# Optimization experiments

Measured on AMD Instinct MI355X. Metric: run time of the kernel, lower is better.

The kernel has to match this reference:

```python
import jax, jax.numpy as jnp
import numpy as np

B, S, D = 2, 2048, 512
H = 8
G = 4
LAMBDA_INIT = 0.2  # 0.8 - 0.6*exp(-0.3*(layer_idx-1)) with layer_idx=1
EPS = 1e-5


def setup_inputs() -> dict:
    key = jax.random.key(0)
    ks = jax.random.split(key, 16)
    n = jax.random.normal
    return {
        "x": n(ks[0], (B, S, D), jnp.float32),
        "K1_w": n(ks[1], (D, D), jnp.float32) * 0.02,
        "K1_b": n(ks[2], (D,), jnp.float32) * 0.02,
        "Q1_w": n(ks[3], (D, D), jnp.float32) * 0.02,
        "K2_w": n(ks[4], (D, D), jnp.float32) * 0.02,
        "K2_b": n(ks[5], (D,), jnp.float32) * 0.02,
        "Q2_w": n(ks[6], (D, D), jnp.float32) * 0.02,
        "V_w": n(ks[7], (D, D), jnp.float32) * 0.02,
        "lambda_q1": n(ks[8], (H, 1), jnp.float32),
        "lambda_k1": n(ks[9], (H, 1), jnp.float32),
        "lambda_q2": n(ks[10], (H, 1), jnp.float32),
        "lambda_k2": n(ks[11], (H, 1), jnp.float32),
        "gn_w": jnp.ones((D,), jnp.float32),
        "gn_b": jnp.zeros((D,), jnp.float32),
        "out_w": n(ks[12], (D, D), jnp.float32) * 0.02,
        "out_b": n(ks[13], (D,), jnp.float32) * 0.02,
    }


def reference(x, K1_w, K1_b, Q1_w, K2_w, K2_b, Q2_w, V_w,
              lambda_q1, lambda_k1, lambda_q2, lambda_k2,
              gn_w, gn_b, out_w, out_b):
    b, s, d = x.shape
    hd = d // H

    def heads(t):  # (b,s,d) -> (b,H,s,hd)
        return t.reshape(b, s, H, hd).transpose(0, 2, 1, 3)

    q1 = heads(x @ Q1_w.T)
    k1 = heads(x @ K1_w.T + K1_b)
    q2 = heads(x @ Q2_w.T)
    k2 = heads(x @ K2_w.T + K2_b)
    v = heads(x @ V_w.T)

    scale = hd ** 0.5
    a1 = jax.nn.softmax(jnp.einsum('bhqd,bhkd->bhqk', q1, k1) / scale, axis=-1)
    a2 = jax.nn.softmax(jnp.einsum('bhqd,bhkd->bhqk', q2, k2) / scale, axis=-1)

    lam = (jnp.exp(lambda_q1 * lambda_k1)
           - jnp.exp(lambda_q2 * lambda_k2) + LAMBDA_INIT)  # (H,1)
    attn = a1 - lam.reshape(1, H, 1, 1) * a2

    o = jnp.einsum('bhqk,bhkd->bhqd', attn, v)
    o = o.transpose(0, 2, 1, 3).reshape(b, s, d)

    # GroupNorm over channels: input (b, d, s), groups G normalize over (d/G, s)
    xc = o.transpose(0, 2, 1).reshape(b, G, d // G, s)
    mu = xc.mean(axis=(2, 3), keepdims=True)
    var = xc.var(axis=(2, 3), keepdims=True)
    xn = ((xc - mu) * jax.lax.rsqrt(var + EPS)).reshape(b, d, s)
    xn = xn * gn_w[None, :, None] + gn_b[None, :, None]

    y = xn.transpose(0, 2, 1) @ out_w.T + out_b
    return y
```

## Files before the change

kernel.cpp:

```cpp
#include <hip/hip_runtime.h>
#include <hip/hip_bf16.h>

typedef __bf16 bf16;
typedef __attribute__((ext_vector_type(8))) __bf16 bf16x8;
typedef __attribute__((ext_vector_type(4))) float f32x4;

#define MFMA16(a, b, c) __builtin_amdgcn_mfma_f32_16x16x32_bf16((a), (b), (c), 0, 0, 0)

static constexpr float EPS = 1e-5f;
static constexpr float LAMBDA_INIT = 0.2f;

__device__ __forceinline__ bf16x8 cvt8(const float* p) {
    const f32x4 a = *(const f32x4*)p;
    const f32x4 b = *(const f32x4*)(p + 4);
    bf16x8 r;
    r[0] = (bf16)a[0]; r[1] = (bf16)a[1]; r[2] = (bf16)a[2]; r[3] = (bf16)a[3];
    r[4] = (bf16)b[0]; r[5] = (bf16)b[1]; r[6] = (bf16)b[2]; r[7] = (bf16)b[3];
    return r;
}

__device__ __forceinline__ void gload_lds16(const void* g, void* l) {
    __builtin_amdgcn_global_load_lds(
        (const __attribute__((address_space(1))) unsigned int*)g,
        (__attribute__((address_space(3))) unsigned int*)l,
        16, 0, 0);
}

__global__ __launch_bounds__(256) void prep_kernel(
    const float* __restrict__ x,
    const float* __restrict__ q1w, const float* __restrict__ k1w,
    const float* __restrict__ q2w, const float* __restrict__ k2w,
    const float* __restrict__ vw,
    const float* __restrict__ ow, const float* __restrict__ gnw,
    const float* __restrict__ gnb,
    bf16* __restrict__ xb, bf16* __restrict__ wb,
    bf16* __restrict__ owg, float* __restrict__ S0, float* __restrict__ stats)
{
    const int tid = threadIdx.x;
    if (blockIdx.x < 1664) {
        const size_t base = ((size_t)blockIdx.x * 256 + tid) * 8;
        if (base < 2097152) {
            *(bf16x8*)(xb + base) = cvt8(x + base);
        } else {
            const size_t wbase = base - 2097152;
            const int wsel = (int)(wbase >> 18);
            const size_t off = wbase & 262143;
            const float* W = (wsel == 0) ? q1w : (wsel == 1) ? k1w :
                             (wsel == 2) ? q2w : (wsel == 3) ? k2w : vw;
            *(bf16x8*)(wb + wbase) = cvt8(W + off);
        }
        return;
    }

    __shared__ float red[4];
    const int pb = blockIdx.x - 1664;
    if (pb == 0 && tid < 16) stats[tid] = 0.f;

    const int n0 = pb * 16;
    const int c0 = tid, c1 = tid + 256;
    const float gw0 = gnw[c0], gw1 = gnw[c1];
    const float gb0 = gnb[c0], gb1 = gnb[c1];

    for (int n = 0; n < 16; ++n) {
        const size_t rowb = (size_t)(n0 + n) * 512;
        const float w0 = ow[rowb + c0];
        const float w1 = ow[rowb + c1];
        owg[rowb + c0] = (bf16)(w0 * gw0);
        owg[rowb + c1] = (bf16)(w1 * gw1);
        float s = gb0 * w0 + gb1 * w1;
#pragma unroll
        for (int off = 1; off < 64; off <<= 1) s += __shfl_xor(s, off, 64);
        if ((tid & 63) == 0) red[tid >> 6] = s;
        __syncthreads();
        if (tid == 0) S0[n0 + n] = red[0] + red[1] + red[2] + red[3];
        __syncthreads();
    }
}

__global__ __launch_bounds__(256) void proj_kernel(
    const bf16* __restrict__ xb, const bf16* __restrict__ wb,
    const float* __restrict__ k1b, const float* __restrict__ k2b,
    bf16* __restrict__ q1o, bf16* __restrict__ k1o,
    bf16* __restrict__ q2o, bf16* __restrict__ k2o,
    bf16* __restrict__ vto)
{
    __shared__ __align__(16) bf16 As[128 * 32];
    __shared__ __align__(16) bf16 Bs[128 * 32];

    const int tid = threadIdx.x;
    const int wave = tid >> 6, lane = tid & 63;
    const int l15 = lane & 15, quad = lane >> 4;
    const int wm = wave >> 1, wn = wave & 1;

    const int mb = blockIdx.x / 20;
    const int nb = blockIdx.x % 20;
    const int wsel = nb >> 2;
    const int nrow0 = (nb & 3) * 128;

    const int srow = lane >> 2;
    const int scol = (lane & 3) * 8;
    const bf16* ag = xb + (size_t)(mb * 128 + srow) * 512 + scol;
    const bf16* bg = wb + (size_t)(wsel * 512 + nrow0 + srow) * 512 + scol;

    f32x4 acc[4][4];
#pragma unroll
    for (int i = 0; i < 4; ++i)
#pragma unroll
        for (int j = 0; j < 4; ++j)
            acc[i][j] = (f32x4){0.f, 0.f, 0.f, 0.f};

    for (int k0 = 0; k0 < 512; k0 += 32) {
#pragma unroll
        for (int c = 0; c < 2; ++c) {
            const int chunk = wave * 2 + c;
            gload_lds16(ag + (size_t)(chunk * 16) * 512 + k0, As + chunk * 512);
            gload_lds16(bg + (size_t)(chunk * 16) * 512 + k0, Bs + chunk * 512);
        }
        __syncthreads();

        bf16x8 af[4], bfr[4];
#pragma unroll
        for (int i = 0; i < 4; ++i)
            af[i] = *(const bf16x8*)(As + (wm * 64 + i * 16 + l15) * 32 + quad * 8);
#pragma unroll
        for (int j = 0; j < 4; ++j)
            bfr[j] = *(const bf16x8*)(Bs + (wn * 64 + j * 16 + l15) * 32 + quad * 8);

#pragma unroll
        for (int i = 0; i < 4; ++i)
#pragma unroll
            for (int j = 0; j < 4; ++j)
                acc[i][j] = MFMA16(af[i], bfr[j], acc[i][j]);

        __syncthreads();
    }

    const float scale = (wsel == 0 || wsel == 2) ? 0.125f : 1.0f;
#pragma unroll
    for (int j = 0; j < 4; ++j) {
        const int ncol = nrow0 + wn * 64 + j * 16 + l15;
        float bias = 0.f;
        if (wsel == 1) bias = k1b[ncol];
        if (wsel == 3) bias = k2b[ncol];
        const int h = ncol >> 6, hd = ncol & 63;
#pragma unroll
        for (int i = 0; i < 4; ++i) {
#pragma unroll
            for (int r = 0; r < 4; ++r) {
                const int m = mb * 128 + wm * 64 + i * 16 + quad * 4 + r;
                const int bidx = m >> 11, s = m & 2047;
                const float v = acc[i][j][r] * scale + bias;
                if (wsel == 4) {
                    const int s5 = s & 31;
                    const int p = ((s5 & 15) >> 2) * 8 + (s5 & 3) + ((s5 >> 4) << 2);
                    const int sp = (s & ~31) | p;
                    vto[((size_t)(bidx * 8 + h) * 64 + hd) * 2048 + sp] = (bf16)v;
                } else {
                    bf16* dst = (wsel == 0) ? q1o : (wsel == 1) ? k1o :
                                (wsel == 2) ? q2o : k2o;
                    dst[((size_t)(bidx * 8 + h) * 2048 + s) * 64 + hd] = (bf16)v;
                }
            }
        }
    }
}

__global__ __launch_bounds__(512, 4) void attn_kernel(
    const bf16* __restrict__ q1, const bf16* __restrict__ k1,
    const bf16* __restrict__ q2, const bf16* __restrict__ k2,
    const bf16* __restrict__ vt,
    const float* __restrict__ lq1, const float* __restrict__ lk1,
    const float* __restrict__ lq2, const float* __restrict__ lk2,
    bf16* __restrict__ o, float* __restrict__ stats)
{
    __shared__ __align__(16) bf16 smem[12288];
    __shared__ float lbuf[8][2][16];
    __shared__ float sred[8][2];

    const int tid = threadIdx.x;
    const int wave = tid >> 6;
    const int lane = tid & 63;
    const int l15 = lane & 15, quad = lane >> 4;
    const int qtile = wave & 3;
    const int kg = wave >> 2;

    const int bh = blockIdx.x >> 5;
    const int qt = blockIdx.x & 31;
    const int b = bh >> 3, h = bh & 7;

    const bf16* k1t = k1 + (size_t)bh * 2048 * 64;
    const bf16* k2t = k2 + (size_t)bh * 2048 * 64;
    const bf16* vtt = vt + (size_t)bh * 64 * 2048;

    const int qrow = qt * 64 + qtile * 16 + l15;
    const bf16* q1p = q1 + ((size_t)bh * 2048 + qrow) * 64 + quad * 8;
    const bf16* q2p = q2 + ((size_t)bh * 2048 + qrow) * 64 + quad * 8;
    const bf16x8 q1f0 = *(const bf16x8*)(q1p);
    const bf16x8 q1f1 = *(const bf16x8*)(q1p + 32);
    const bf16x8 q2f0 = *(const bf16x8*)(q2p);
    const bf16x8 q2f1 = *(const bf16x8*)(q2p + 32);

    const int sw = wave & 3;
    const int skey0 = (wave < 4) ? 0 : 1024;
    bf16* k1dst = smem + wave * 512;
    bf16* k2dst = smem + 4096 + wave * 512;
    bf16* vdst  = smem + 8192 + wave * 512;
    const size_t ksrc0 = (size_t)(skey0 + sw * 8 + (lane >> 3)) * 64
                       + 8 * ((lane & 7) ^ (lane >> 3));
    const size_t vsrc0 = (size_t)(sw * 16 + (lane >> 2)) * 2048 + skey0 + (lane & 3) * 8;

    const bf16* k1r = smem + kg * 2048;
    const bf16* k2r = smem + 4096 + kg * 2048;
    const bf16* vr  = smem + 8192 + kg * 2048;

    const int koffa = 8 * (quad ^ (l15 & 7));
    const int koffb = 8 * ((quad + 4) ^ (l15 & 7));

    f32x4 O1[4], O2[4];
    float l1 = 0.f, l2 = 0.f;
#pragma unroll
    for (int t = 0; t < 4; ++t) {
        O1[t] = (f32x4){0.f, 0.f, 0.f, 0.f};
        O2[t] = (f32x4){0.f, 0.f, 0.f, 0.f};
    }

    for (int it = 0; it < 32; ++it) {
        const size_t koff = ksrc0 + (size_t)it * 32 * 64;
        gload_lds16(k1t + koff, k1dst);
        gload_lds16(k2t + koff, k2dst);
        gload_lds16(vtt + vsrc0 + it * 32, vdst);
        __syncthreads();

        const bf16x8 k1t0a = *(const bf16x8*)(k1r + l15 * 64 + koffa);
        const bf16x8 k1t0b = *(const bf16x8*)(k1r + l15 * 64 + koffb);
        const bf16x8 k1t1a = *(const bf16x8*)(k1r + (16 + l15) * 64 + koffa);
        const bf16x8 k1t1b = *(const bf16x8*)(k1r + (16 + l15) * 64 + koffb);
        const bf16x8 k2t0a = *(const bf16x8*)(k2r + l15 * 64 + koffa);
        const bf16x8 k2t0b = *(const bf16x8*)(k2r + l15 * 64 + koffb);
        const bf16x8 k2t1a = *(const bf16x8*)(k2r + (16 + l15) * 64 + koffa);
        const bf16x8 k2t1b = *(const bf16x8*)(k2r + (16 + l15) * 64 + koffb);
        const bf16x8 v0 = *(const bf16x8*)(vr + l15 * 32 + quad * 8);
        const bf16x8 v1 = *(const bf16x8*)(vr + (16 + l15) * 32 + quad * 8);
        const bf16x8 v2 = *(const bf16x8*)(vr + (32 + l15) * 32 + quad * 8);
        const bf16x8 v3 = *(const bf16x8*)(vr + (48 + l15) * 32 + quad * 8);

        f32x4 z = (f32x4){0.f, 0.f, 0.f, 0.f};
        f32x4 s1t0 = MFMA16(k1t0a, q1f0, z);  s1t0 = MFMA16(k1t0b, q1f1, s1t0);
        f32x4 s1t1 = MFMA16(k1t1a, q1f0, z);  s1t1 = MFMA16(k1t1b, q1f1, s1t1);
        f32x4 s2t0 = MFMA16(k2t0a, q2f0, z);  s2t0 = MFMA16(k2t0b, q2f1, s2t0);
        f32x4 s2t1 = MFMA16(k2t1a, q2f0, z);  s2t1 = MFMA16(k2t1b, q2f1, s2t1);

        bf16x8 b1, b2;
#pragma unroll
        for (int r = 0; r < 4; ++r) {
            float e;
            e = __expf(s1t0[r]); l1 += e; b1[r]     = (bf16)e;
            e = __expf(s1t1[r]); l1 += e; b1[4 + r] = (bf16)e;
            e = __expf(s2t0[r]); l2 += e; b2[r]     = (bf16)e;
            e = __expf(s2t1[r]); l2 += e; b2[4 + r] = (bf16)e;
        }

        O1[0] = MFMA16(v0, b1, O1[0]);
        O1[1] = MFMA16(v1, b1, O1[1]);
        O1[2] = MFMA16(v2, b1, O1[2]);
        O1[3] = MFMA16(v3, b1, O1[3]);
        O2[0] = MFMA16(v0, b2, O2[0]);
        O2[1] = MFMA16(v1, b2, O2[1]);
        O2[2] = MFMA16(v2, b2, O2[2]);
        O2[3] = MFMA16(v3, b2, O2[3]);

        __syncthreads();
    }

    l1 += __shfl_xor(l1, 16, 64);  l1 += __shfl_xor(l1, 32, 64);
    l2 += __shfl_xor(l2, 16, 64);  l2 += __shfl_xor(l2, 32, 64);
    if (lane < 16) {
        lbuf[wave][0][lane] = l1;
        lbuf[wave][1][lane] = l2;
    }
    __syncthreads();

    f32x4* rb = (f32x4*)smem;
    if (wave == 4 || wave == 5) {
        f32x4* dst = rb + (wave - 4) * 512;
#pragma unroll
        for (int t = 0; t < 4; ++t) {
            dst[t * 64 + lane]       = O1[t];
            dst[(4 + t) * 64 + lane] = O2[t];
        }
    }
    __syncthreads();
    if (wave == 0 || wave == 1) {
        const f32x4* src = rb + wave * 512;
#pragma unroll
        for (int t = 0; t < 4; ++t) {
            O1[t] += src[t * 64 + lane];
            O2[t] += src[(4 + t) * 64 + lane];
        }
    }
    __syncthreads();
    if (wave == 6 || wave == 7) {
        f32x4* dst = rb + (wave - 6) * 512;
#pragma unroll
        for (int t = 0; t < 4; ++t) {
            dst[t * 64 + lane]       = O1[t];
            dst[(4 + t) * 64 + lane] = O2[t];
        }
    }
    __syncthreads();
    if (wave == 2 || wave == 3) {
        const f32x4* src = rb + (wave - 2) * 512;
#pragma unroll
        for (int t = 0; t < 4; ++t) {
            O1[t] += src[t * 64 + lane];
            O2[t] += src[(4 + t) * 64 + lane];
        }
    }

    float ssum = 0.f, ssq = 0.f;
    if (wave < 4) {
        const float L1 = l1 + lbuf[wave + 4][0][l15];
        const float L2 = l2 + lbuf[wave + 4][1][l15];
        const float lam = __expf(lq1[h] * lk1[h]) - __expf(lq2[h] * lk2[h]) + LAMBDA_INIT;
        const float inv1 = 1.f / L1;
        const float inv2 = lam / L2;
        const size_t row = (size_t)(b * 2048 + qt * 64 + wave * 16 + l15) * 512 + h * 64;
#pragma unroll
        for (int t = 0; t < 4; ++t) {
#pragma unroll
            for (int r = 0; r < 4; ++r) {
                const float val = O1[t][r] * inv1 - O2[t][r] * inv2;
                ssum += val;
                ssq += val * val;
                o[row + t * 16 + quad * 4 + r] = (bf16)val;
            }
        }
    }
#pragma unroll
    for (int off = 1; off < 64; off <<= 1) {
        ssum += __shfl_xor(ssum, off, 64);
        ssq += __shfl_xor(ssq, off, 64);
    }
    if (lane == 0) { sred[wave][0] = ssum; sred[wave][1] = ssq; }
    __syncthreads();
    if (tid == 0) {
        float s0 = 0.f, s1 = 0.f;
        for (int w = 0; w < 8; ++w) { s0 += sred[w][0]; s1 += sred[w][1]; }
        const int bg = b * 4 + (h >> 1);
        atomicAdd(&stats[bg * 2], s0);
        atomicAdd(&stats[bg * 2 + 1], s1);
    }
}

__global__ __launch_bounds__(256) void out_gemm_kernel(
    const bf16* __restrict__ o, const bf16* __restrict__ owg,
    const float* __restrict__ S0, const float* __restrict__ stats,
    const float* __restrict__ ob, float* __restrict__ y)
{
    __shared__ __align__(16) bf16 As[64 * 32];
    __shared__ __align__(16) bf16 Bs[64 * 32];

    const int tid = threadIdx.x;
    const int wave = tid >> 6, lane = tid & 63;
    const int l15 = lane & 15, quad = lane >> 4;

    const int mb = blockIdx.x >> 3;
    const int nb = blockIdx.x & 7;
    const int b = mb >> 5;

    const float N = 128.f * 2048.f;
    float mu[4], rs[4];
#pragma unroll
    for (int g = 0; g < 4; ++g) {
        const float m = stats[(b * 4 + g) * 2] / N;
        const float var = stats[(b * 4 + g) * 2 + 1] / N - m * m;
        mu[g] = m;
        rs[g] = rsqrtf(var + EPS);
    }

    const int srow = wave * 16 + (lane >> 2);
    const int scol = (lane & 3) * 8;
    const bf16* ag = o + (size_t)(mb * 64 + srow) * 512 + scol;
    const bf16* bg = owg + (size_t)(nb * 64 + srow) * 512 + scol;
    bf16* adst = As + wave * 512;
    bf16* bdst = Bs + wave * 512;

    f32x4 acc[4], tot[4];
#pragma unroll
    for (int i = 0; i < 4; ++i) {
        acc[i] = (f32x4){0.f, 0.f, 0.f, 0.f};
        tot[i] = (f32x4){0.f, 0.f, 0.f, 0.f};
    }
    float s1g[4];
    float s1p = 0.f;
#pragma unroll
    for (int g = 0; g < 4; ++g) s1g[g] = 0.f;

    for (int kk = 0; kk < 16; ++kk) {
        gload_lds16(ag + kk * 32, adst);
        gload_lds16(bg + kk * 32, bdst);
        __syncthreads();

        bf16x8 af[4];
#pragma unroll
        for (int i = 0; i < 4; ++i)
            af[i] = *(const bf16x8*)(As + (i * 16 + l15) * 32 + quad * 8);
        const bf16x8 bf = *(const bf16x8*)(Bs + (wave * 16 + l15) * 32 + quad * 8);

#pragma unroll
        for (int i = 0; i < 4; ++i)
            acc[i] = MFMA16(af[i], bf, acc[i]);

#pragma unroll
        for (int j = 0; j < 8; ++j) s1p += (float)bf[j];

        __syncthreads();

        if ((kk & 3) == 3) {
            const int g = kk >> 2;
#pragma unroll
            for (int i = 0; i < 4; ++i) {
#pragma unroll
                for (int r = 0; r < 4; ++r) tot[i][r] += rs[g] * acc[i][r];
                acc[i] = (f32x4){0.f, 0.f, 0.f, 0.f};
            }
            float sg = s1p + __shfl_xor(s1p, 16, 64);
            sg += __shfl_xor(sg, 32, 64);
            s1g[g] = sg;
            s1p = 0.f;
        }
    }

    const int ncol = nb * 64 + wave * 16 + l15;
    float bias = S0[ncol] + ob[ncol];
#pragma unroll
    for (int g = 0; g < 4; ++g) bias -= mu[g] * rs[g] * s1g[g];

#pragma unroll
    for (int i = 0; i < 4; ++i) {
#pragma unroll
        for (int r = 0; r < 4; ++r) {
            const int m = mb * 64 + i * 16 + quad * 4 + r;
            y[(size_t)m * 512 + ncol] = tot[i][r] + bias;
        }
    }
}

extern "C" void kernel_launch(void* const* d_in, const int* in_sizes, int n_in,
                              void* d_out, int out_size, void* d_ws, size_t ws_size,
                              hipStream_t stream)
{
    const float* x   = (const float*)d_in[0];
    const float* K1w = (const float*)d_in[1];
    const float* K1b = (const float*)d_in[2];
    const float* Q1w = (const float*)d_in[3];
    const float* K2w = (const float*)d_in[4];
    const float* K2b = (const float*)d_in[5];
    const float* Q2w = (const float*)d_in[6];
    const float* Vw  = (const float*)d_in[7];
    const float* lq1 = (const float*)d_in[8];
    const float* lk1 = (const float*)d_in[9];
    const float* lq2 = (const float*)d_in[10];
    const float* lk2 = (const float*)d_in[11];
    const float* gnw = (const float*)d_in[12];
    const float* gnb = (const float*)d_in[13];
    const float* Ow  = (const float*)d_in[14];
    const float* Ob  = (const float*)d_in[15];

    const size_t SZ = (size_t)2 * 8 * 2048 * 64;
    bf16* q1 = (bf16*)d_ws;
    bf16* k1 = q1 + SZ;
    bf16* q2 = k1 + SZ;
    bf16* k2 = q2 + SZ;
    bf16* vt = k2 + SZ;
    bf16* o  = vt + SZ;
    bf16* xb = o;
    bf16* wb = o + SZ;
    bf16* owg = wb + (size_t)2560 * 512;
    float* S0 = (float*)(owg + 512 * 512);
    float* stats = S0 + 512;

    prep_kernel<<<1696, 256, 0, stream>>>(x, Q1w, K1w, Q2w, K2w, Vw,
                                          Ow, gnw, gnb, xb, wb, owg, S0, stats);
    proj_kernel<<<640, 256, 0, stream>>>(xb, wb, K1b, K2b,
                                         q1, k1, q2, k2, vt);
    attn_kernel<<<512, 512, 0, stream>>>(q1, k1, q2, k2, vt,
                                         lq1, lk1, lq2, lk2, o, stats);
    out_gemm_kernel<<<512, 256, 0, stream>>>(o, owg, S0, stats, Ob,
                                             (float*)d_out);
}
```

Baseline: 190.2 us.

## Fuse four kernels into one persistent kernel with atomic grid barriers

Merges the prep, projection, attention and output GEMM kernels into a single 512-block, 512-thread kernel. The stages are separated by software grid-wide barriers built on atomic counters, which are reset by a memset before the launch. This is meant to remove three kernel-launch gaps and their tail drain. In exchange the projection GEMM is reshaped to 8 waves with 128 tiles spread over 512 blocks, so some blocks do two tiles, and half the waves sit idle in the output GEMM. The barriers assume all 512 blocks are resident at once; otherwise the kernel deadlocks.

After: 456.3 us. +139.9%, slower.

```diff
diff --git a/kernel.cpp b/kernel.cpp
--- a/kernel.cpp
+++ b/kernel.cpp
@@ -9,6 +9,7 @@
 
 static constexpr float EPS = 1e-5f;
 static constexpr float LAMBDA_INIT = 0.2f;
+static constexpr unsigned NBLK = 512;
 
 __device__ __forceinline__ bf16x8 cvt8(const float* p) {
     const f32x4 a = *(const f32x4*)p;
@@ -26,422 +27,407 @@
         16, 0, 0);
 }
 
-__global__ __launch_bounds__(256) void prep_kernel(
+__device__ __forceinline__ void grid_sync(unsigned* cnt) {
+    __syncthreads();
+    if (threadIdx.x == 0) {
+        __threadfence();
+        __hip_atomic_fetch_add(cnt, 1u, __ATOMIC_ACQ_REL, __HIP_MEMORY_SCOPE_AGENT);
+        while (__hip_atomic_load(cnt, __ATOMIC_ACQUIRE, __HIP_MEMORY_SCOPE_AGENT) < NBLK)
+            __builtin_amdgcn_s_sleep(8);
+        __threadfence();
+    }
+    __syncthreads();
+}
+
+__global__ __launch_bounds__(512, 4) void mega_kernel(
     const float* __restrict__ x,
     const float* __restrict__ q1w, const float* __restrict__ k1w,
     const float* __restrict__ q2w, const float* __restrict__ k2w,
     const float* __restrict__ vw,
+    const float* __restrict__ k1b, const float* __restrict__ k2b,
+    const float* __restrict__ lq1, const float* __restrict__ lk1,
+    const float* __restrict__ lq2, const float* __restrict__ lk2,
     const float* __restrict__ ow, const float* __restrict__ gnw,
-    const float* __restrict__ gnb,
+    const float* __restrict__ gnb, const float* __restrict__ ob,
     bf16* __restrict__ xb, bf16* __restrict__ wb,
-    bf16* __restrict__ owg, float* __restrict__ S0, float* __restrict__ stats)
+    bf16* __restrict__ q1, bf16* __restrict__ k1,
+    bf16* __restrict__ q2, bf16* __restrict__ k2,
+    bf16* __restrict__ vt, bf16* __restrict__ o,
+    bf16* __restrict__ owg, float* __restrict__ S0,
+    float* __restrict__ stats, unsigned* __restrict__ bar,
+    float* __restrict__ y)
 {
+    __shared__ __align__(16) bf16 smem[12288];
+    __shared__ float lbuf[8][2][16];
+    __shared__ float sred[8][2];
+
     const int tid = threadIdx.x;
-    if (blockIdx.x < 1664) {
-        const size_t base = ((size_t)blockIdx.x * 256 + tid) * 8;
-        if (base < 2097152) {
+    const int wave = tid >> 6;
+    const int lane = tid & 63;
+    const int l15 = lane & 15, quad = lane >> 4;
+
+    {
+        const unsigned gtid = blockIdx.x * 512 + tid;
+        {
+            const size_t base = (size_t)gtid * 8;
             *(bf16x8*)(xb + base) = cvt8(x + base);
-        } else {
-            const size_t wbase = base - 2097152;
+        }
+        if (gtid < 163840u) {
+            const size_t wbase = (size_t)gtid * 8;
             const int wsel = (int)(wbase >> 18);
             const size_t off = wbase & 262143;
             const float* W = (wsel == 0) ? q1w : (wsel == 1) ? k1w :
                              (wsel == 2) ? q2w : (wsel == 3) ? k2w : vw;
             *(bf16x8*)(wb + wbase) = cvt8(W + off);
         }
-        return;
+        const int n = blockIdx.x;
+        const float w = ow[(size_t)n * 512 + tid];
+        owg[(size_t)n * 512 + tid] = (bf16)(w * gnw[tid]);
+        float s = gnb[tid] * w;
+#pragma unroll
+        for (int off = 1; off < 64; off <<= 1) s += __shfl_xor(s, off, 64);
+        if (lane == 0) sred[wave][0] = s;
+        __syncthreads();
+        if (tid == 0) {
+            float t0 = 0.f;
+            for (int wv = 0; wv < 8; ++wv) t0 += sred[wv][0];
+            S0[n] = t0;
+        }
+        if (blockIdx.x == 0 && tid < 16) stats[tid] = 0.f;
     }
-
-    __shared__ float red[4];
-    const int pb = blockIdx.x - 1664;
-    if (pb == 0 && tid < 16) stats[tid] = 0.f;
-
-    const int n0 = pb * 16;
-    const int c0 = tid, c1 = tid + 256;
-    const float gw0 = gnw[c0], gw1 = gnw[c1];
-    const float gb0 = gnb[c0], gb1 = gnb[c1];
-
-    for (int n = 0; n < 16; ++n) {
-        const size_t rowb = (size_t)(n0 + n) * 512;
-        const float w0 = ow[rowb + c0];
-        const float w1 = ow[rowb + c1];
-        owg[rowb + c0] = (bf16)(w0 * gw0);
-        owg[rowb + c1] = (bf16)(w1 * gw1);
-        float s = gb0 * w0 + gb1 * w1;
-#pragma unroll
-        for (int off = 1; off < 64; off <<= 1) s += __shfl_xor(s, off, 64);
-        if ((tid & 63) == 0) red[tid >> 6] = s;
-        __syncthreads();
-        if (tid == 0) S0[n0 + n] = red[0] + red[1] + red[2] + red[3];
-        __syncthreads();
+    grid_sync(bar + 0);
+
+    {
+        bf16* As = smem;
+        bf16* Bs = smem + 4096;
+        const int wm = wave >> 2, wn = wave & 3;
+        const int srow = lane >> 2;
+        const int scol = (lane & 3) * 8;
+
+        for (int t = blockIdx.x; t < 640; t += 512) {
+            const int mb = t / 20;
+            const int nb = t % 20;
+            const int wsel = nb >> 2;
+            const int nrow0 = (nb & 3) * 128;
+
+            const bf16* ag = xb + (size_t)(mb * 128 + srow) * 512 + scol;
+            const bf16* bg = wb + (size_t)(wsel * 512 + nrow0 + srow) * 512 + scol;
+
+            f32x4 acc[4][2];
+#pragma unroll
+            for (int i = 0; i < 4; ++i)
+#pragma unroll
+                for (int j = 0; j < 2; ++j)
+                    acc[i][j] = (f32x4){0.f, 0.f, 0.f, 0.f};
+
+            for (int k0 = 0; k0 < 512; k0 += 32) {
+                gload_lds16(ag + (size_t)(wave * 16) * 512 + k0, As + wave * 512);
+                gload_lds16(bg + (size_t)(wave * 16) * 512 + k0, Bs + wave * 512);
+                __syncthreads();
+
+                bf16x8 af[4], bfr[2];
+#pragma unroll
+                for (int i = 0; i < 4; ++i)
+                    af[i] = *(const bf16x8*)(As + (wm * 64 + i * 16 + l15) * 32 + quad * 8);
+#pragma unroll
+                for (int j = 0; j < 2; ++j)
+                    bfr[j] = *(const bf16x8*)(Bs + (wn * 32 + j * 16 + l15) * 32 + quad * 8);
+
+#pragma unroll
+                for (int i = 0; i < 4; ++i)
+#pragma unroll
+                    for (int j = 0; j < 2; ++j)
+                        acc[i][j] = MFMA16(af[i], bfr[j], acc[i][j]);
+
+                __syncthreads();
+            }
+
+            const float scale = (wsel == 0 || wsel == 2) ? 0.125f : 1.0f;
+#pragma unroll
+            for (int j = 0; j < 2; ++j) {
+                const int ncol = nrow0 + wn * 32 + j * 16 + l15;
+                float bias = 0.f;
+                if (wsel == 1) bias = k1b[ncol];
+                if (wsel == 3) bias = k2b[ncol];
+                const int h = ncol >> 6, hd = ncol & 63;
+#pragma unroll
+                for (int i = 0; i < 4; ++i) {
+#pragma unroll
+                    for (int r = 0; r < 4; ++r) {
+                        const int m = mb * 128 + wm * 64 + i * 16 + quad * 4 + r;
+                        const int bidx = m >> 11, s = m & 2047;
+                        const float v = acc[i][j][r] * scale + bias;
+                        if (wsel == 4) {
+                            const int s5 = s & 31;
+                            const int p = ((s5 & 15) >> 2) * 8 + (s5 & 3) + ((s5 >> 4) << 2);
+                            const int sp = (s & ~31) | p;
+                            vt[((size_t)(bidx * 8 + h) * 64 + hd) * 2048 + sp] = (bf16)v;
+                        } else {
+                            bf16* dst = (wsel == 0) ? q1 : (wsel == 1) ? k1 :
+                                        (wsel == 2) ? q2 : k2;
+                            dst[((size_t)(bidx * 8 + h) * 2048 + s) * 64 + hd] = (bf16)v;
+                        }
+                    }
+                }
+            }
+        }
     }
-}
-
-__global__ __launch_bounds__(256) void proj_kernel(
-    const bf16* __restrict__ xb, const bf16* __restrict__ wb,
-    const float* __restrict__ k1b, const float* __restrict__ k2b,
-    bf16* __restrict__ q1o, bf16* __restrict__ k1o,
-    bf16* __restrict__ q2o, bf16* __restrict__ k2o,
-    bf16* __restrict__ vto)
-{
-    __shared__ __align__(16) bf16 As[128 * 32];
-    __shared__ __align__(16) bf16 Bs[128 * 32];
-
-    const int tid = threadIdx.x;
-    const int wave = tid >> 6, lane = tid & 63;
-    const int l15 = lane & 15, quad = lane >> 4;
-    const int wm = wave >> 1, wn = wave & 1;
-
-    const int mb = blockIdx.x / 20;
-    const int nb = blockIdx.x % 20;
-    const int wsel = nb >> 2;
-    const int nrow0 = (nb & 3) * 128;
-
-    const int srow = lane >> 2;
-    const int scol = (lane & 3) * 8;
-    const bf16* ag = xb + (size_t)(mb * 128 + srow) * 512 + scol;
-    const bf16* bg = wb + (size_t)(wsel * 512 + nrow0 + srow) * 512 + scol;
-
-    f32x4 acc[4][4];
-#pragma unroll
-    for (int i = 0; i < 4; ++i)
-#pragma unroll
-        for (int j = 0; j < 4; ++j)
-            acc[i][j] = (f32x4){0.f, 0.f, 0.f, 0.f};
-
-    for (int k0 = 0; k0 < 512; k0 += 32) {
-#pragma unroll
-        for (int c = 0; c < 2; ++c) {
-            const int chunk = wave * 2 + c;
-            gload_lds16(ag + (size_t)(chunk * 16) * 512 + k0, As + chunk * 512);
-            gload_lds16(bg + (size_t)(chunk * 16) * 512 + k0, Bs + chunk * 512);
-        }
-        __syncthreads();
-
-        bf16x8 af[4], bfr[4];
-#pragma unroll
-        for (int i = 0; i < 4; ++i)
-            af[i] = *(const bf16x8*)(As + (wm * 64 + i * 16 + l15) * 32 + quad * 8);
-#pragma unroll
-        for (int j = 0; j < 4; ++j)
-            bfr[j] = *(const bf16x8*)(Bs + (wn * 64 + j * 16 + l15) * 32 + quad * 8);
-
-#pragma unroll
-        for (int i = 0; i < 4; ++i)
-#pragma unroll
-            for (int j = 0; j < 4; ++j)
-                acc[i][j] = MFMA16(af[i], bfr[j], acc[i][j]);
-
-        __syncthreads();
+    grid_sync(bar + 1);
+
+    {
+        const int qtile = wave & 3;
+        const int kg = wave >> 2;
+        const int bh = blockIdx.x >> 5;
+        const int qt = blockIdx.x & 31;
+        const int b = bh >> 3, h = bh & 7;
+
+        const bf16* k1t = k1 + (size_t)bh * 2048 * 64;
+        const bf16* k2t = k2 + (size_t)bh * 2048 * 64;
+        const bf16* vtt = vt + (size_t)bh * 64 * 2048;
+
+        const int qrow = qt * 64 + qtile * 16 + l15;
+        const bf16* q1p = q1 + ((size_t)bh * 2048 + qrow) * 64 + quad * 8;
+        const bf16* q2p = q2 + ((size_t)bh * 2048 + qrow) * 64 + quad * 8;
+        const bf16x8 q1f0 = *(const bf16x8*)(q1p);
+        const bf16x8 q1f1 = *(const bf16x8*)(q1p + 32);
+        const bf16x8 q2f0 = *(const bf16x8*)(q2p);
+        const bf16x8 q2f1 = *(const bf16x8*)(q2p + 32);
+
+        const int sw = wave & 3;
+        const int skey0 = (wave < 4) ? 0 : 1024;
+        bf16* k1dst = smem + wave * 512;
+        bf16* k2dst = smem + 4096 + wave * 512;
+        bf16* vdst  = smem + 8192 + wave * 512;
+        const size_t ksrc0 = (size_t)(skey0 + sw * 8 + (lane >> 3)) * 64
+                           + 8 * ((lane & 7) ^ (lane >> 3));
+        const size_t vsrc0 = (size_t)(sw * 16 + (lane >> 2)) * 2048 + skey0 + (lane & 3) * 8;
+
+        const bf16* k1r = smem + kg * 2048;
+        const bf16* k2r = smem + 4096 + kg * 2048;
+        const bf16* vr  = smem + 8192 + kg * 2048;
+        const int koffa = 8 * (quad ^ (l15 & 7));
+        const int koffb = 8 * ((quad + 4) ^ (l15 & 7));
+
+        f32x4 O1[4], O2[4];
+        float l1 = 0.f, l2 = 0.f;
+#pragma unroll
+        for (int t = 0; t < 4; ++t) {
+            O1[t] = (f32x4){0.f, 0.f, 0.f, 0.f};
+            O2[t] = (f32x4){0.f, 0.f, 0.f, 0.f};
+        }
+
+        for (int it = 0; it < 32; ++it) {
+            const size_t koff = ksrc0 + (size_t)it * 32 * 64;
+            gload_lds16(k1t + koff, k1dst);
+            gload_lds16(k2t + koff, k2dst);
+            gload_lds16(vtt + vsrc0 + it * 32, vdst);
+            __syncthreads();
+
+            const bf16x8 k1t0a = *(const bf16x8*)(k1r + l15 * 64 + koffa);
+            const bf16x8 k1t0b = *(const bf16x8*)(k1r + l15 * 64 + koffb);
+            const bf16x8 k1t1a = *(const bf16x8*)(k1r + (16 + l15) * 64 + koffa);
+            const bf16x8 k1t1b = *(const bf16x8*)(k1r + (16 + l15) * 64 + koffb);
+            const bf16x8 k2t0a = *(const bf16x8*)(k2r + l15 * 64 + koffa);
+            const bf16x8 k2t0b = *(const bf16x8*)(k2r + l15 * 64 + koffb);
+            const bf16x8 k2t1a = *(const bf16x8*)(k2r + (16 + l15) * 64 + koffa);
+            const bf16x8 k2t1b = *(const bf16x8*)(k2r + (16 + l15) * 64 + koffb);
+            const bf16x8 v0 = *(const bf16x8*)(vr + l15 * 32 + quad * 8);
+            const bf16x8 v1 = *(const bf16x8*)(vr + (16 + l15) * 32 + quad * 8);
+            const bf16x8 v2 = *(const bf16x8*)(vr + (32 + l15) * 32 + quad * 8);
+            const bf16x8 v3 = *(const bf16x8*)(vr + (48 + l15) * 32 + quad * 8);
+
+            f32x4 z = (f32x4){0.f, 0.f, 0.f, 0.f};
+            f32x4 s1t0 = MFMA16(k1t0a, q1f0, z);  s1t0 = MFMA16(k1t0b, q1f1, s1t0);
+            f32x4 s1t1 = MFMA16(k1t1a, q1f0, z);  s1t1 = MFMA16(k1t1b, q1f1, s1t1);
+            f32x4 s2t0 = MFMA16(k2t0a, q2f0, z);  s2t0 = MFMA16(k2t0b, q2f1, s2t0);
+            f32x4 s2t1 = MFMA16(k2t1a, q2f0, z);  s2t1 = MFMA16(k2t1b, q2f1, s2t1);
+
+            bf16x8 b1, b2;
+#pragma unroll
+            for (int r = 0; r < 4; ++r) {
+                float e;
+                e = __expf(s1t0[r]); l1 += e; b1[r]     = (bf16)e;
+                e = __expf(s1t1[r]); l1 += e; b1[4 + r] = (bf16)e;
+                e = __expf(s2t0[r]); l2 += e; b2[r]     = (bf16)e;
+                e = __expf(s2t1[r]); l2 += e; b2[4 + r] = (bf16)e;
+            }
+
+            O1[0] = MFMA16(v0, b1, O1[0]);
+            O1[1] = MFMA16(v1, b1, O1[1]);
+            O1[2] = MFMA16(v2, b1, O1[2]);
+            O1[3] = MFMA16(v3, b1, O1[3]);
+            O2[0] = MFMA16(v0, b2, O2[0]);
+            O2[1] = MFMA16(v1, b2, O2[1]);
+            O2[2] = MFMA16(v2, b2, O2[2]);
+            O2[3] = MFMA16(v3, b2, O2[3]);
+
+            __syncthreads();
+        }
+
+        l1 += __shfl_xor(l1, 16, 64);  l1 += __shfl_xor(l1, 32, 64);
+        l2 += __shfl_xor(l2, 16, 64);  l2 += __shfl_xor(l2, 32, 64);
+        if (lane < 16) {
+            lbuf[wave][0][lane] = l1;
+            lbuf[wave][1][lane] = l2;
+        }
+        __syncthreads();
+
+        f32x4* rb = (f32x4*)smem;
+        if (wave == 4 || wave == 5) {
+            f32x4* dst = rb + (wave - 4) * 512;
+#pragma unroll
+            for (int t = 0; t < 4; ++t) {
+                dst[t * 64 + lane]       = O1[t];
+                dst[(4 + t) * 64 + lane] = O2[t];
+            }
+        }
+        __syncthreads();
+        if (wave == 0 || wave == 1) {
+            const f32x4* src = rb + wave * 512;
+#pragma unroll
+            for (int t = 0; t < 4; ++t) {
+                O1[t] += src[t * 64 + lane];
+                O2[t] += src[(4 + t) * 64 + lane];
+            }
+        }
+        __syncthreads();
+        if (wave == 6 || wave == 7) {
+            f32x4* dst = rb + (wave - 6) * 512;
+#pragma unroll
+            for (int t = 0; t < 4; ++t) {
+                dst[t * 64 + lane]       = O1[t];
+                dst[(4 + t) * 64 + lane] = O2[t];
+            }
+        }
+        __syncthreads();
+        if (wave == 2 || wave == 3) {
+            const f32x4* src = rb + (wave - 2) * 512;
+#pragma unroll
+            for (int t = 0; t < 4; ++t) {
+                O1[t] += src[t * 64 + lane];
+                O2[t] += src[(4 + t) * 64 + lane];
+            }
+        }
+
+        float ssum = 0.f, ssq = 0.f;
+        if (wave < 4) {
+            const float L1 = l1 + lbuf[wave + 4][0][l15];
+            const float L2 = l2 + lbuf[wave + 4][1][l15];
+            const float lam = __expf(lq1[h] * lk1[h]) - __expf(lq2[h] * lk2[h]) + LAMBDA_INIT;
+            const float inv1 = 1.f / L1;
+            const float inv2 = lam / L2;
+            const size_t row = (size_t)(b * 2048 + qt * 64 + wave * 16 + l15) * 512 + h * 64;
+#pragma unroll
+            for (int t = 0; t < 4; ++t) {
+#pragma unroll
+                for (int r = 0; r < 4; ++r) {
+                    const float val = O1[t][r] * inv1 - O2[t][r] * inv2;
+                    ssum += val;
+                    ssq += val * val;
+                    o[row + t * 16 + quad * 4 + r] = (bf16)val;
+                }
+            }
+        }
+#pragma unroll
+        for (int off = 1; off < 64; off <<= 1) {
+            ssum += __shfl_xor(ssum, off, 64);
+            ssq += __shfl_xor(ssq, off, 64);
+        }
+        if (lane == 0) { sred[wave][0] = ssum; sred[wave][1] = ssq; }
+        __syncthreads();
+        if (tid == 0) {
+            float s0 = 0.f, s1 = 0.f;
+            for (int wv = 0; wv < 8; ++wv) { s0 += sred[wv][0]; s1 += sred[wv][1]; }
+            const int bg = b * 4 + (h >> 1);
+            atomicAdd(&stats[bg * 2], s0);
+            atomicAdd(&stats[bg * 2 + 1], s1);
+        }
     }
-
-    const float scale = (wsel == 0 || wsel == 2) ? 0.125f : 1.0f;
-#pragma unroll
-    for (int j = 0; j < 4; ++j) {
-        const int ncol = nrow0 + wn * 64 + j * 16 + l15;
-        float bias = 0.f;
-        if (wsel == 1) bias = k1b[ncol];
-        if (wsel == 3) bias = k2b[ncol];
-        const int h = ncol >> 6, hd = ncol & 63;
+    grid_sync(bar + 2);
+
+    {
+        bf16* As = smem;
+        bf16* Bs = smem + 2048;
+        const int mb = blockIdx.x >> 3;
+        const int nb = blockIdx.x & 7;
+        const int b = mb >> 5;
+
+        const float N = 128.f * 2048.f;
+        float mu[4], rs[4];
+#pragma unroll
+        for (int g = 0; g < 4; ++g) {
+            const float m = stats[(b * 4 + g) * 2] / N;
+            const float var = stats[(b * 4 + g) * 2 + 1] / N - m * m;
+            mu[g] = m;
+            rs[g] = rsqrtf(var + EPS);
+        }
+
+        const int srow = wave * 16 + (lane >> 2);
+        const int scol = (lane & 3) * 8;
+        const bf16* ag = o + (size_t)(mb * 64 + srow) * 512 + scol;
+        const bf16* bg = owg + (size_t)(nb * 64 + srow) * 512 + scol;
+        bf16* adst = As + wave * 512;
+        bf16* bdst = Bs + wave * 512;
+
+        f32x4 acc[4], tot[4];
 #pragma unroll
         for (int i = 0; i < 4; ++i) {
-#pragma unroll
-            for (int r = 0; r < 4; ++r) {
-                const int m = mb * 128 + wm * 64 + i * 16 + quad * 4 + r;
-                const int bidx = m >> 11, s = m & 2047;
-                const float v = acc[i][j][r] * scale + bias;
-                if (wsel == 4) {
-                    const int s5 = s & 31;
-                    const int p = ((s5 & 15) >> 2) * 8 + (s5 & 3) + ((s5 >> 4) << 2);
-                    const int sp = (s & ~31) | p;
-                    vto[((size_t)(bidx * 8 + h) * 64 + hd) * 2048 + sp] = (bf16)v;
-                } else {
-                    bf16* dst = (wsel == 0) ? q1o : (wsel == 1) ? k1o :
-                                (wsel == 2) ? q2o : k2o;
-                    dst[((size_t)(bidx * 8 + h) * 2048 + s) * 64 + hd] = (bf16)v;
+            acc[i] = (f32x4){0.f, 0.f, 0.f, 0.f};
+            tot[i] = (f32x4){0.f, 0.f, 0.f, 0.f};
+        }
+        float s1g[4] = {0.f, 0.f, 0.f, 0.f};
+        float s1p = 0.f;
+
+        for (int kk = 0; kk < 16; ++kk) {
+            if (wave < 4) {
+                gload_lds16(ag + kk * 32, adst);
+                gload_lds16(bg + kk * 32, bdst);
+            }
+            __syncthreads();
+
+            if (wave < 4) {
+                bf16x8 af[4];
+#pragma unroll
+                for (int i = 0; i < 4; ++i)
+                    af[i] = *(const bf16x8*)(As + (i * 16 + l15) * 32 + quad * 8);
+                const bf16x8 bfv = *(const bf16x8*)(Bs + (wave * 16 + l15) * 32 + quad * 8);
+
+#pragma unroll
+                for (int i = 0; i < 4; ++i)
+                    acc[i] = MFMA16(af[i], bfv, acc[i]);
+#pragma unroll
+                for (int j = 0; j < 8; ++j) s1p += (float)bfv[j];
+            }
+            __syncthreads();
+
+            if (wave < 4 && (kk & 3) == 3) {
+                const int g = kk >> 2;
+#pragma unroll
+                for (int i = 0; i < 4; ++i) {
+#pragma unroll
+                    for (int r = 0; r < 4; ++r) tot[i][r] += rs[g] * acc[i][r];
+                    acc[i] = (f32x4){0.f, 0.f, 0.f, 0.f};
                 }
-            }
-        }
-    }
-}
-
-__global__ __launch_bounds__(512, 4) void attn_kernel(
-    const bf16* __restrict__ q1, const bf16* __restrict__ k1,
-    const bf16* __restrict__ q2, const bf16* __restrict__ k2,
-    const bf16* __restrict__ vt,
-    const float* __restrict__ lq1, const float* __restrict__ lk1,
-    const float* __restrict__ lq2, const float* __restrict__ lk2,
-    bf16* __restrict__ o, float* __restrict__ stats)
-{
-    __shared__ __align__(16) bf16 smem[12288];
-    __shared__ float lbuf[8][2][16];
-    __shared__ float sred[8][2];
-
-    const int tid = threadIdx.x;
-    const int wave = tid >> 6;
-    const int lane = tid & 63;
-    const int l15 = lane & 15, quad = lane >> 4;
-    const int qtile = wave & 3;
-    const int kg = wave >> 2;
-
-    const int bh = blockIdx.x >> 5;
-    const int qt = blockIdx.x & 31;
-    const int b = bh >> 3, h = bh & 7;
-
-    const bf16* k1t = k1 + (size_t)bh * 2048 * 64;
-    const bf16* k2t = k2 + (size_t)bh * 2048 * 64;
-    const bf16* vtt = vt + (size_t)bh * 64 * 2048;
-
-    const int qrow = qt * 64 + qtile * 16 + l15;
-    const bf16* q1p = q1 + ((size_t)bh * 2048 + qrow) * 64 + quad * 8;
-    const bf16* q2p = q2 + ((size_t)bh * 2048 + qrow) * 64 + quad * 8;
-    const bf16x8 q1f0 = *(const bf16x8*)(q1p);
-    const bf16x8 q1f1 = *(const bf16x8*)(q1p + 32);
-    const bf16x8 q2f0 = *(const bf16x8*)(q2p);
-    const bf16x8 q2f1 = *(const bf16x8*)(q2p + 32);
-
-    const int sw = wave & 3;
-    const int skey0 = (wave < 4) ? 0 : 1024;
-    bf16* k1dst = smem + wave * 512;
-    bf16* k2dst = smem + 4096 + wave * 512;
-    bf16* vdst  = smem + 8192 + wave * 512;
-    const size_t ksrc0 = (size_t)(skey0 + sw * 8 + (lane >> 3)) * 64
-                       + 8 * ((lane & 7) ^ (lane >> 3));
-    const size_t vsrc0 = (size_t)(sw * 16 + (lane >> 2)) * 2048 + skey0 + (lane & 3) * 8;
-
-    const bf16* k1r = smem + kg * 2048;
-    const bf16* k2r = smem + 4096 + kg * 2048;
-    const bf16* vr  = smem + 8192 + kg * 2048;
-
-    const int koffa = 8 * (quad ^ (l15 & 7));
-    const int koffb = 8 * ((quad + 4) ^ (l15 & 7));
-
-    f32x4 O1[4], O2[4];
-    float l1 = 0.f, l2 = 0.f;
-#pragma unroll
-    for (int t = 0; t < 4; ++t) {
-        O1[t] = (f32x4){0.f, 0.f, 0.f, 0.f};
-        O2[t] = (f32x4){0.f, 0.f, 0.f, 0.f};
-    }
-
-    for (int it = 0; it < 32; ++it) {
-        const size_t koff = ksrc0 + (size_t)it * 32 * 64;
-        gload_lds16(k1t + koff, k1dst);
-        gload_lds16(k2t + koff, k2dst);
-        gload_lds16(vtt + vsrc0 + it * 32, vdst);
-        __syncthreads();
-
-        const bf16x8 k1t0a = *(const bf16x8*)(k1r + l15 * 64 + koffa);
-        const bf16x8 k1t0b = *(const bf16x8*)(k1r + l15 * 64 + koffb);
-        const bf16x8 k1t1a = *(const bf16x8*)(k1r + (16 + l15) * 64 + koffa);
-        const bf16x8 k1t1b = *(const bf16x8*)(k1r + (16 + l15) * 64 + koffb);
-        const bf16x8 k2t0a = *(const bf16x8*)(k2r + l15 * 64 + koffa);
-        const bf16x8 k2t0b = *(const bf16x8*)(k2r + l15 * 64 + koffb);
-        const bf16x8 k2t1a = *(const bf16x8*)(k2r + (16 + l15) * 64 + koffa);
-        const bf16x8 k2t1b = *(const bf16x8*)(k2r + (16 + l15) * 64 + koffb);
-        const bf16x8 v0 = *(const bf16x8*)(vr + l15 * 32 + quad * 8);
-        const bf16x8 v1 = *(const bf16x8*)(vr + (16 + l15) * 32 + quad * 8);
-        const bf16x8 v2 = *(const bf16x8*)(vr + (32 + l15) * 32 + quad * 8);
-        const bf16x8 v3 = *(const bf16x8*)(vr + (48 + l15) * 32 + quad * 8);
-
-        f32x4 z = (f32x4){0.f, 0.f, 0.f, 0.f};
-        f32x4 s1t0 = MFMA16(k1t0a, q1f0, z);  s1t0 = MFMA16(k1t0b, q1f1, s1t0);
-        f32x4 s1t1 = MFMA16(k1t1a, q1f0, z);  s1t1 = MFMA16(k1t1b, q1f1, s1t1);
-        f32x4 s2t0 = MFMA16(k2t0a, q2f0, z);  s2t0 = MFMA16(k2t0b, q2f1, s2t0);
-        f32x4 s2t1 = MFMA16(k2t1a, q2f0, z);  s2t1 = MFMA16(k2t1b, q2f1, s2t1);
-
-        bf16x8 b1, b2;
-#pragma unroll
-        for (int r = 0; r < 4; ++r) {
-            float e;
-            e = __expf(s1t0[r]); l1 += e; b1[r]     = (bf16)e;
-            e = __expf(s1t1[r]); l1 += e; b1[4 + r] = (bf16)e;
-            e = __expf(s2t0[r]); l2 += e; b2[r]     = (bf16)e;
-            e = __expf(s2t1[r]); l2 += e; b2[4 + r] = (bf16)e;
-        }
-
-        O1[0] = MFMA16(v0, b1, O1[0]);
-        O1[1] = MFMA16(v1, b1, O1[1]);
-        O1[2] = MFMA16(v2, b1, O1[2]);
-        O1[3] = MFMA16(v3, b1, O1[3]);
-        O2[0] = MFMA16(v0, b2, O2[0]);
-        O2[1] = MFMA16(v1, b2, O2[1]);
-        O2[2] = MFMA16(v2, b2, O2[2]);
-        O2[3] = MFMA16(v3, b2, O2[3]);
-
-        __syncthreads();
-    }
-
-    l1 += __shfl_xor(l1, 16, 64);  l1 += __shfl_xor(l1, 32, 64);
-    l2 += __shfl_xor(l2, 16, 64);  l2 += __shfl_xor(l2, 32, 64);
-    if (lane < 16) {
-        lbuf[wave][0][lane] = l1;
-        lbuf[wave][1][lane] = l2;
-    }
-    __syncthreads();
-
-    f32x4* rb = (f32x4*)smem;
-    if (wave == 4 || wave == 5) {
-        f32x4* dst = rb + (wave - 4) * 512;
-#pragma unroll
-        for (int t = 0; t < 4; ++t) {
-            dst[t * 64 + lane]       = O1[t];
-            dst[(4 + t) * 64 + lane] = O2[t];
-        }
-    }
-    __syncthreads();
-    if (wave == 0 || wave == 1) {
-        const f32x4* src = rb + wave * 512;
-#pragma unroll
-        for (int t = 0; t < 4; ++t) {
-            O1[t] += src[t * 64 + lane];
-            O2[t] += src[(4 + t) * 64 + lane];
-        }
-    }
-    __syncthreads();
-    if (wave == 6 || wave == 7) {
-        f32x4* dst = rb + (wave - 6) * 512;
-#pragma unroll
-        for (int t = 0; t < 4; ++t) {
-            dst[t * 64 + lane]       = O1[t];
-            dst[(4 + t) * 64 + lane] = O2[t];
-        }
-    }
-    __syncthreads();
-    if (wave == 2 || wave == 3) {
-        const f32x4* src = rb + (wave - 2) * 512;
-#pragma unroll
-        for (int t = 0; t < 4; ++t) {
-            O1[t] += src[t * 64 + lane];
-            O2[t] += src[(4 + t) * 64 + lane];
-        }
-    }
-
-    float ssum = 0.f, ssq = 0.f;
-    if (wave < 4) {
-        const float L1 = l1 + lbuf[wave + 4][0][l15];
-        const float L2 = l2 + lbuf[wave + 4][1][l15];
-        const float lam = __expf(lq1[h] * lk1[h]) - __expf(lq2[h] * lk2[h]) + LAMBDA_INIT;
-        const float inv1 = 1.f / L1;
-        const float inv2 = lam / L2;
-        const size_t row = (size_t)(b * 2048 + qt * 64 + wave * 16 + l15) * 512 + h * 64;
-#pragma unroll
-        for (int t = 0; t < 4; ++t) {
-#pragma unroll
-            for (int r = 0; r < 4; ++r) {
-                const float val = O1[t][r] * inv1 - O2[t][r] * inv2;
-                ssum += val;
-                ssq += val * val;
-                o[row + t * 16 + quad * 4 + r] = (bf16)val;
-            }
-        }
-    }
-#pragma unroll
-    for (int off = 1; off < 64; off <<= 1) {
-        ssum += __shfl_xor(ssum, off, 64);
-        ssq += __shfl_xor(ssq, off, 64);
-    }
-    if (lane == 0) { sred[wave][0] = ssum; sred[wave][1] = ssq; }
-    __syncthreads();
-    if (tid == 0) {
-        float s0 = 0.f, s1 = 0.f;
-        for (int w = 0; w < 8; ++w) { s0 += sred[w][0]; s1 += sred[w][1]; }
-        const int bg = b * 4 + (h >> 1);
-        atomicAdd(&stats[bg * 2], s0);
-        atomicAdd(&stats[bg * 2 + 1], s1);
-    }
-}
-
-__global__ __launch_bounds__(256) void out_gemm_kernel(
-    const bf16* __restrict__ o, const bf16* __restrict__ owg,
-    const float* __restrict__ S0, const float* __restrict__ stats,
-    const float* __restrict__ ob, float* __restrict__ y)
-{
-    __shared__ __align__(16) bf16 As[64 * 32];
-    __shared__ __align__(16) bf16 Bs[64 * 32];
-
-    const int tid = threadIdx.x;
-    const int wave = tid >> 6, lane = tid & 63;
-    const int l15 = lane & 15, quad = lane >> 4;
-
-    const int mb = blockIdx.x >> 3;
-    const int nb = blockIdx.x & 7;
-    const int b = mb >> 5;
-
-    const float N = 128.f * 2048.f;
-    float mu[4], rs[4];
-#pragma unroll
-    for (int g = 0; g < 4; ++g) {
-        const float m = stats[(b * 4 + g) * 2] / N;
-        const float var = stats[(b * 4 + g) * 2 + 1] / N - m * m;
-        mu[g] = m;
-        rs[g] = rsqrtf(var + EPS);
-    }
-
-    const int srow = wave * 16 + (lane >> 2);
-    const int scol = (lane & 3) * 8;
-    const bf16* ag = o + (size_t)(mb * 64 + srow) * 512 + scol;
-    const bf16* bg = owg + (size_t)(nb * 64 + srow) * 512 + scol;
-    bf16* adst = As + wave * 512;
-    bf16* bdst = Bs + wave * 512;
-
-    f32x4 acc[4], tot[4];
-#pragma unroll
-    for (int i = 0; i < 4; ++i) {
-        acc[i] = (f32x4){0.f, 0.f, 0.f, 0.f};
-        tot[i] = (f32x4){0.f, 0.f, 0.f, 0.f};
-    }
-    float s1g[4];
-    float s1p = 0.f;
-#pragma unroll
-    for (int g = 0; g < 4; ++g) s1g[g] = 0.f;
-
-    for (int kk = 0; kk < 16; ++kk) {
-        gload_lds16(ag + kk * 32, adst);
-        gload_lds16(bg + kk * 32, bdst);
-        __syncthreads();
-
-        bf16x8 af[4];
-#pragma unroll
-        for (int i = 0; i < 4; ++i)
-            af[i] = *(const bf16x8*)(As + (i * 16 + l15) * 32 + quad * 8);
-        const bf16x8 bf = *(const bf16x8*)(Bs + (wave * 16 + l15) * 32 + quad * 8);
-
-#pragma unroll
-        for (int i = 0; i < 4; ++i)
-            acc[i] = MFMA16(af[i], bf, acc[i]);
-
-#pragma unroll
-        for (int j = 0; j < 8; ++j) s1p += (float)bf[j];
-
-        __syncthreads();
-
-        if ((kk & 3) == 3) {
-            const int g = kk >> 2;
+                float sg = s1p + __shfl_xor(s1p, 16, 64);
+                sg += __shfl_xor(sg, 32, 64);
+                s1g[g] = sg;
+                s1p = 0.f;
+            }
+        }
+
+        if (wave < 4) {
+            const int ncol = nb * 64 + wave * 16 + l15;
+            float bias = S0[ncol] + ob[ncol];
+#pragma unroll
+            for (int g = 0; g < 4; ++g) bias -= mu[g] * rs[g] * s1g[g];
 #pragma unroll
             for (int i = 0; i < 4; ++i) {
 #pragma unroll
-                for (int r = 0; r < 4; ++r) tot[i][r] += rs[g] * acc[i][r];
-                acc[i] = (f32x4){0.f, 0.f, 0.f, 0.f};
-            }
-            float sg = s1p + __shfl_xor(s1p, 16, 64);
-            sg += __shfl_xor(sg, 32, 64);
-            s1g[g] = sg;
-            s1p = 0.f;
-        }
-    }
-
-    const int ncol = nb * 64 + wave * 16 + l15;
-    float bias = S0[ncol] + ob[ncol];
-#pragma unroll
-    for (int g = 0; g < 4; ++g) bias -= mu[g] * rs[g] * s1g[g];
-
-#pragma unroll
-    for (int i = 0; i < 4; ++i) {
-#pragma unroll
-        for (int r = 0; r < 4; ++r) {
-            const int m = mb * 64 + i * 16 + quad * 4 + r;
-            y[(size_t)m * 512 + ncol] = tot[i][r] + bias;
+                for (int r = 0; r < 4; ++r) {
+                    const int m = mb * 64 + i * 16 + quad * 4 + r;
+                    y[(size_t)m * 512 + ncol] = tot[i][r] + bias;
+                }
+            }
         }
     }
 }
@@ -479,13 +465,12 @@
     bf16* owg = wb + (size_t)2560 * 512;
     float* S0 = (float*)(owg + 512 * 512);
     float* stats = S0 + 512;
-
-    prep_kernel<<<1696, 256, 0, stream>>>(x, Q1w, K1w, Q2w, K2w, Vw,
-                                          Ow, gnw, gnb, xb, wb, owg, S0, stats);
-    proj_kernel<<<640, 256, 0, stream>>>(xb, wb, K1b, K2b,
-                                         q1, k1, q2, k2, vt);
-    attn_kernel<<<512, 512, 0, stream>>>(q1, k1, q2, k2, vt,
-                                         lq1, lk1, lq2, lk2, o, stats);
-    out_gemm_kernel<<<512, 256, 0, stream>>>(o, owg, S0, stats, Ob,
-                                             (float*)d_out);
+    unsigned* bar = (unsigned*)(stats + 16);
+
+    hipMemsetAsync(bar, 0, 3 * sizeof(unsigned), stream);
+    mega_kernel<<<512, 512, 0, stream>>>(
+        x, Q1w, K1w, Q2w, K2w, Vw, K1b, K2b,
+        lq1, lk1, lq2, lk2, Ow, gnw, gnb, Ob,
+        xb, wb, q1, k1, q2, k2, vt, o, owg, S0, stats, bar,
+        (float*)d_out);
 }
```
